# Performance work log

Hardware: AMD Instinct MI355X
Metric: run time of the kernel (lower is better)

The kernel has to match this reference:

```python
import jax, jax.numpy as jnp
import numpy as np

ROUTING_ITER = 2
EPS = 1e-8


def squash(s, axis):
    # s * ||s||^2 / (1 + ||s||^2) / ||s||
    sq = jnp.sum(s * s, axis=axis, keepdims=True)
    return s * (sq / (1.0 + sq)) / jnp.sqrt(sq + EPS)


def setup_inputs() -> dict:
    key = jax.random.key(0)
    k1, k2 = jax.random.split(key)
    B, N_in, d_in = 64, 2048, 16
    J, D = 32, 16  # num_capsule, dim_capsule
    x = jax.random.normal(k1, (B, N_in, 1, d_in), dtype=jnp.float32)
    weight = jax.random.normal(k2, (1, N_in, J, D, d_in), dtype=jnp.float32) * 0.05
    return {"x": x, "weight": weight}


def reference(x, weight):
    # x: [B, N_in, 1, d_in]; weight: [1, N_in, J, D, d_in]
    # prediction vectors u[b,i,j,:] = W[i,j] @ x[b,i]
    u = jnp.einsum('ijde,bie->bijd', weight[0], x[:, :, 0, :])  # [B,N_in,J,D]
    B, N_in, J, D = u.shape

    # dynamic routing on stop_gradient(u)
    u_sg = jax.lax.stop_gradient(u)
    b = jnp.zeros((B, N_in, J, 1), dtype=u.dtype)
    for _ in range(ROUTING_ITER):
        c = jax.nn.softmax(b, axis=2)                      # [B,N_in,J,1]
        s = jnp.sum(u_sg * c, axis=1, keepdims=True)       # [B,1,J,D]
        v = squash(s, axis=2)                              # squash over capsule axis (faithful)
        b = b + jnp.sum(u_sg * v, axis=-1, keepdims=True)  # [B,N_in,J,1]

    c = jax.nn.softmax(b, axis=2)
    s = jnp.sum(u * c, axis=1)  # [B,J,D]
    return squash(s, axis=-1)
```

## Files before the change

### kernel.cpp

```cpp
#include <hip/hip_runtime.h>

typedef __attribute__((ext_vector_type(8))) short short8;
typedef __attribute__((ext_vector_type(4))) float f32x4;
typedef __attribute__((ext_vector_type(2))) float f32x2;
typedef __attribute__((ext_vector_type(4))) unsigned int uint4v;
typedef unsigned short u16;

#define NI 2048

__device__ __forceinline__ unsigned int packbf2(float a, float b){
  unsigned int ua = __float_as_uint(a), ub = __float_as_uint(b);
  unsigned int ra = (ua + 0x7FFFu + ((ua >> 16) & 1u)) >> 16;
  unsigned int rb = (ub + 0x7FFFu + ((ub >> 16) & 1u)) & 0xFFFF0000u;
  return ra | rb;
}
__device__ __forceinline__ float bflo(unsigned int p){ return __uint_as_float(p << 16); }
__device__ __forceinline__ float bfhi(unsigned int p){ return __uint_as_float(p & 0xFFFF0000u); }

__device__ __forceinline__ uint4v cvt8(const f32x4& a, const f32x4& b){
  uint4v p = { packbf2(a.x, a.y), packbf2(a.z, a.w),
               packbf2(b.x, b.y), packbf2(b.z, b.w) };
  return p;
}

__device__ __forceinline__ void gl_lds16(const void* g, void* l){
  __builtin_amdgcn_global_load_lds(
      (const __attribute__((address_space(1))) unsigned int*)g,
      (__attribute__((address_space(3))) unsigned int*)l, 16, 0, 0);
}

__device__ __forceinline__ f32x4 squash4(const f32x4& q){
  f32x4 f;
  f.x = q.x / ((1.f + q.x) * sqrtf(q.x + 1e-8f));
  f.y = q.y / ((1.f + q.y) * sqrtf(q.y + 1e-8f));
  f.z = q.z / ((1.f + q.z) * sqrtf(q.z + 1e-8f));
  f.w = q.w / ((1.f + q.w) * sqrtf(q.w + 1e-8f));
  return f;
}


#define FUSED_SMEM 156672

template<int MODE>
__device__ __forceinline__ void pass_phase(
    const u16* __restrict__ sW, const u16* __restrict__ sX,
    float* __restrict__ sSumA, float* __restrict__ sSumB,
    const float* __restrict__ Sv1, const float* __restrict__ qv1,
    const float* __restrict__ Sv2, const float* __restrict__ qv2,
    float* __restrict__ partials, int blk, int t)
{
  const int w = t >> 6, lane = t & 63;
  const int wtile = w & 1, jhalf = (w >> 1) & 1, bh = w >> 2;
  const int lq = lane >> 4, lb = lane & 15, qs = lq & 1;
  const int bg = bh * 32 + wtile * 16 + lb;
  const short8 zero8 = {0,0,0,0,0,0,0,0};
  const f32x4 zf4 = {0.f,0.f,0.f,0.f};

  f32x4 acc[16];
  #pragma unroll
  for (int tj = 0; tj < 16; ++tj) acc[tj] = zf4;

  unsigned int vpl[16], vph[16];
  if constexpr (MODE >= 1){
    f32x4 qa = *(const f32x4*)(qv1 + bg * 16 + lq * 4);
    f32x4 fa = squash4(qa);
    f32x4 fb = zf4;
    if constexpr (MODE == 2){
      f32x4 qb = *(const f32x4*)(qv2 + bg * 16 + lq * 4);
      fb = squash4(qb);
    }
    #pragma unroll
    for (int tj = 0; tj < 16; ++tj){
      int jd = (jhalf * 16 + tj) * 16 + lq * 4;
      f32x4 sv = *(const f32x4*)(Sv1 + bg * 512 + jd);
      f32x4 v;
      v.x = sv.x * fa.x; v.y = sv.y * fa.y; v.z = sv.z * fa.z; v.w = sv.w * fa.w;
      if constexpr (MODE == 2){
        f32x4 s2 = *(const f32x4*)(Sv2 + bg * 512 + jd);
        v.x += s2.x * fb.x; v.y += s2.y * fb.y; v.z += s2.z * fb.z; v.w += s2.w * fb.w;
      }
      vpl[tj] = packbf2(v.x, v.y);
      vph[tj] = packbf2(v.z, v.w);
    }
  }

  if constexpr (MODE == 0){
    const int rsel = lq >> 1;
    #pragma unroll
    for (int s = 0; s < 4; ++s){
      const u16* wrow = sW + (size_t)(2 * s + rsel) * 8192;
      const u16* xrow = sX + (size_t)(2 * s + rsel) * 1024;
      short8 bfrag = *(const short8*)(xrow + bg * 16 + qs * 8);
      #pragma unroll
      for (int tj = 0; tj < 16; ++tj){
        int j = jhalf * 16 + tj;
        short8 afrag = *(const short8*)(wrow + j * 256 + lb * 16 + qs * 8);
        acc[tj] = __builtin_amdgcn_mfma_f32_16x16x32_bf16(afrag, bfrag, acc[tj], 0, 0, 0);
      }
    }
  } else {
    for (int s = 0; s < 8; ++s){
      const u16* wrow = sW + (size_t)s * 8192;
      const u16* xrow = sX + (size_t)s * 1024;
      short8 bl8 = *(const short8*)(xrow + bg * 16 + qs * 8);
      short8 bfrag = (lq < 2) ? bl8 : zero8;
      f32x4 ut[16];
      float e[16];
      float ps = 0.f;
      #pragma unroll
      for (int tj = 0; tj < 16; ++tj){
        int j = jhalf * 16 + tj;
        short8 afrag = *(const short8*)(wrow + j * 256 + lb * 16 + qs * 8);
        ut[tj] = __builtin_amdgcn_mfma_f32_16x16x32_bf16(afrag, bfrag, zf4, 0, 0, 0);
        float p = ut[tj].x * bflo(vpl[tj]) + ut[tj].y * bfhi(vpl[tj])
                + ut[tj].z * bflo(vph[tj]) + ut[tj].w * bfhi(vph[tj]);
        p += __shfl_xor(p, 16, 64);
        p += __shfl_xor(p, 32, 64);
        e[tj] = __expf(p);
        ps += e[tj];
      }
      float* sS = (s & 1) ? sSumB : sSumA;
      if (lane < 16) sS[w * 16 + lane] = ps;
      __syncthreads();
      float inv = 1.0f / (ps + sS[(w ^ 2) * 16 + lb]);
      #pragma unroll
      for (int tj = 0; tj < 16; ++tj){
        float c = e[tj] * inv;
        acc[tj].x += c * ut[tj].x;
        acc[tj].y += c * ut[tj].y;
        acc[tj].z += c * ut[tj].z;
        acc[tj].w += c * ut[tj].w;
      }
    }
  }

  float* dst = partials + ((size_t)blk * 8 + (size_t)w) * 4096 + (size_t)lane * 64;
  #pragma unroll
  for (int tj = 0; tj < 16; ++tj) *(f32x4*)(dst + tj * 4) = acc[tj];
}

__device__ __forceinline__ void reduce_phase(
    const float* __restrict__ partials, float* __restrict__ S,
    float* __restrict__ qbd, float* __restrict__ qbj,
    float scale, f32x4* __restrict__ sRed4, int blk, int t)
{
  const int qd = t & 31;
  const int dg = t >> 5;
  const float* src = partials + (size_t)dg * 16 * 32768 + (size_t)blk * 128 + qd * 4;
  f32x4 ld[16];
  #pragma unroll
  for (int p = 0; p < 16; ++p) ld[p] = *(const f32x4*)(src + (size_t)p * 32768);
  f32x4 a = ld[0];
  #pragma unroll
  for (int p = 1; p < 16; ++p){ a.x += ld[p].x; a.y += ld[p].y; a.z += ld[p].z; a.w += ld[p].w; }
  sRed4[t] = a;
  __syncthreads();
  if (t < 32){
    f32x4 s = sRed4[t];
    #pragma unroll
    for (int g = 1; g < 16; ++g){
      f32x4 r = sRed4[g * 32 + t];
      s.x += r.x; s.y += r.y; s.z += r.z; s.w += r.w;
    }
    s.x *= scale; s.y *= scale; s.z *= scale; s.w *= scale;
    const int oo = blk * 128 + t * 4;
    const int k = oo & 63, ln = (oo >> 6) & 63, wd = (oo >> 12) & 3, bh = oo >> 14;
    const int b = bh * 32 + (wd & 1) * 16 + (ln & 15);
    const int j = (wd >> 1) * 16 + (k >> 2);
    const int d0 = (ln >> 4) << 2;
    *(f32x4*)(S + b * 512 + j * 16 + d0) = s;
    if (qbd){
      atomicAdd(qbd + b * 16 + d0 + 0, s.x * s.x);
      atomicAdd(qbd + b * 16 + d0 + 1, s.y * s.y);
      atomicAdd(qbd + b * 16 + d0 + 2, s.z * s.z);
      atomicAdd(qbd + b * 16 + d0 + 3, s.w * s.w);
    }
    if (qbj) atomicAdd(qbj + b * 32 + j, s.x * s.x + s.y * s.y + s.z * s.z + s.w * s.w);
  }
  __syncthreads();
}

__global__ __launch_bounds__(512, 2)
void caps_fused(const float* __restrict__ X, const float* __restrict__ W,
                unsigned int* __restrict__ gcnt,
                float* __restrict__ qb1, float* __restrict__ qb2,
                float* __restrict__ qb3,
                float* __restrict__ S1, float* __restrict__ S2, float* __restrict__ S3,
                float* __restrict__ partials, float* __restrict__ out)
{
  extern __shared__ __align__(16) char smem[];
  u16* sW = (u16*)smem;
  u16* sX = (u16*)(smem + 131072);
  float* sSumA = (float*)(smem + 147456);
  float* sSumB = (float*)(smem + 147968);
  f32x4* sRed4 = (f32x4*)(smem + 148480);

  const int t = threadIdx.x;
  const int blk = blockIdx.x;
  const size_t i0 = (size_t)blk * 8;

  {
    const float* wsrc = W + i0 * 8192;
    #pragma unroll
    for (int k = 0; k < 16; ++k){
      int idx = k * 4096 + t * 8;
      f32x4 a = *(const f32x4*)(wsrc + idx);
      f32x4 b = *(const f32x4*)(wsrc + idx + 4);
      *(uint4v*)(sW + idx) = cvt8(a, b);
    }
    int r = t >> 6, b = t & 63;
    const float* xs = X + ((size_t)b * NI + i0 + (size_t)r) * 16;
    f32x4 a0 = *(const f32x4*)(xs);
    f32x4 a1 = *(const f32x4*)(xs + 4);
    f32x4 a2 = *(const f32x4*)(xs + 8);
    f32x4 a3 = *(const f32x4*)(xs + 12);
    *(uint4v*)(sX + t * 16)     = cvt8(a0, a1);
    *(uint4v*)(sX + t * 16 + 8) = cvt8(a2, a3);
  }
  __syncthreads();

  unsigned int gen = 0;
  auto gridsync = [&](bool wait){
    ++gen;
    __syncthreads();
    if (t == 0){
      __builtin_amdgcn_fence(__ATOMIC_RELEASE, "agent");
      __hip_atomic_fetch_add(gcnt + (blk & 7) * 4, 1u,
                             __ATOMIC_RELAXED, __HIP_MEMORY_SCOPE_AGENT);
      if (blk == 0){
        #pragma unroll 1
        for (int g = 0; g < 8; ++g){
          while (__hip_atomic_load(gcnt + g * 4, __ATOMIC_RELAXED,
                                   __HIP_MEMORY_SCOPE_AGENT) < gen * 32u)
            __builtin_amdgcn_s_sleep(2);
        }
        __builtin_amdgcn_fence(__ATOMIC_ACQ_REL, "agent");
        #pragma unroll
        for (int g = 0; g < 8; ++g)
          __hip_atomic_store(gcnt + 64 + g * 64, gen,
                             __ATOMIC_RELAXED, __HIP_MEMORY_SCOPE_AGENT);
      } else if (wait){
        while (__hip_atomic_load(gcnt + 64 + (blk & 7) * 64, __ATOMIC_RELAXED,
                                 __HIP_MEMORY_SCOPE_AGENT) < gen)
          __builtin_amdgcn_s_sleep(2);
        __builtin_amdgcn_fence(__ATOMIC_ACQUIRE, "agent");
      }
    }
    __syncthreads();
  };

  pass_phase<0>(sW, sX, sSumA, sSumB, nullptr, nullptr, nullptr, nullptr, partials, blk, t);
  gridsync(true);
  reduce_phase(partials, S1, qb1, nullptr, 1.0f / 32.0f, sRed4, blk, t);
  gridsync(true);

  pass_phase<1>(sW, sX, sSumA, sSumB, S1, qb1, nullptr, nullptr, partials, blk, t);
  gridsync(true);
  reduce_phase(partials, S2, qb2, nullptr, 1.0f, sRed4, blk, t);
  gridsync(true);

  pass_phase<2>(sW, sX, sSumA, sSumB, S1, qb1, S2, qb2, partials, blk, t);
  gridsync(true);
  reduce_phase(partials, S3, nullptr, qb3, 1.0f, sRed4, blk, t);
  gridsync(blk < 64);

  if (blk < 64){
    float s = S3[blk * 512 + t];
    float q = qb3[blk * 32 + (t >> 4)];
    out[blk * 512 + t] = s * (q / ((1.f + q) * sqrtf(q + 1e-8f)));
  }
}


__global__ __launch_bounds__(256)
void caps_prep(const float* __restrict__ W, const float* __restrict__ X,
               u16* __restrict__ Wb, u16* __restrict__ Xb)
{
  const int bid = blockIdx.x;
  if (bid < 8192){
    size_t base = (size_t)bid * 2048 + (size_t)threadIdx.x * 8;
    f32x4 a = *(const f32x4*)(W + base);
    f32x4 b = *(const f32x4*)(W + base + 4);
    *(uint4v*)(Wb + base) = cvt8(a, b);
  } else {
    int p = (bid - 8192) * 256 + threadIdx.x;
    int i = p >> 6, b = p & 63;
    const float* src = X + ((size_t)b * NI + i) * 16;
    f32x4 a0 = *(const f32x4*)(src);
    f32x4 a1 = *(const f32x4*)(src + 4);
    f32x4 a2 = *(const f32x4*)(src + 8);
    f32x4 a3 = *(const f32x4*)(src + 12);
    *(uint4v*)(Xb + (size_t)p * 16)     = cvt8(a0, a1);
    *(uint4v*)(Xb + (size_t)p * 16 + 8) = cvt8(a2, a3);
  }
}

template<int MODE>
__global__ __launch_bounds__(256, 2)
void caps_pass_f(const u16* __restrict__ Wb,
                 const u16* __restrict__ Xb,
                 const float* __restrict__ vbuf,
                 float* __restrict__ partials, int CI)
{
  constexpr int WR = (MODE == 0) ? 2 : 1;
  __shared__ __align__(16) u16 sW[2][WR * 8192];
  __shared__ __align__(16) u16 sX[2][WR * 512];
  __shared__ float sSum[4][16];

  const int t     = threadIdx.x;
  const int w     = t >> 6;
  const int lane  = t & 63;
  const int wtile = w & 1;
  const int jhalf = w >> 1;
  const int lq    = lane >> 4;
  const int lb    = lane & 15;
  const int q1    = lq & 1;
  const int bhalf = blockIdx.x & 1;
  const int iblk  = blockIdx.x >> 1;
  const int bloc  = wtile * 16 + lb;
  const int bg    = bhalf * 32 + bloc;
  const size_t i0 = (size_t)iblk * (size_t)CI;

  const short8 zero8 = {0,0,0,0,0,0,0,0};
  const f32x4  zf4   = {0.f,0.f,0.f,0.f};

  f32x4 acc[16];
  #pragma unroll
  for (int tj = 0; tj < 16; ++tj) acc[tj] = zf4;

  unsigned int vpl[16], vph[16];
  if constexpr (MODE == 1){
    #pragma unroll
    for (int tj = 0; tj < 16; ++tj){
      f32x4 v = *(const f32x4*)(&vbuf[bg * 512 + (jhalf * 16 + tj) * 16 + lq * 4]);
      vpl[tj] = packbf2(v.x, v.y);
      vph[tj] = packbf2(v.z, v.w);
    }
  }

  auto stage = [&](int nb, size_t irow){
    #pragma unroll
    for (int rr = 0; rr < WR; ++rr){
      const u16* src = Wb + (irow + rr) * 8192 + (size_t)(w * 4) * 512;
      u16* dst = &sW[nb][rr * 8192 + w * 4 * 512];
      #pragma unroll
      for (int r = 0; r < 4; ++r)
        gl_lds16(src + r * 512 + lane * 8, dst + r * 512);
    }
    if (w >= 4 - WR){
      int rr = w - (4 - WR);
      gl_lds16(Xb + ((irow + rr) * 64 + (size_t)bhalf * 32) * 16 + lane * 8,
               &sX[nb][rr * 512]);
    }
  };

  const int NSTEP = CI / WR;
  stage(0, i0);
  __syncthreads();

  for (int s = 0; s < NSTEP; ++s){
    const int buf = s & 1;
    if (s + 1 < NSTEP) stage(buf ^ 1, i0 + (size_t)(s + 1) * WR);

    if constexpr (MODE == 0){
      const int rsel = lq >> 1;
      short8 bfrag = *(const short8*)(&sX[buf][rsel * 512 + bloc * 16 + q1 * 8]);
      #pragma unroll
      for (int tj = 0; tj < 16; ++tj){
        int j = jhalf * 16 + tj;
        short8 afrag = *(const short8*)(&sW[buf][rsel * 8192 + j * 256 + lb * 16 + q1 * 8]);
        acc[tj] = __builtin_amdgcn_mfma_f32_16x16x32_bf16(afrag, bfrag, acc[tj], 0, 0, 0);
      }
    } else {
      short8 bl8 = *(const short8*)(&sX[buf][bloc * 16 + q1 * 8]);
      short8 bfrag = (lq < 2) ? bl8 : zero8;
      f32x4 ut[16];
      float e[16];
      float ps = 0.f;
      #pragma unroll
      for (int tj = 0; tj < 16; ++tj){
        int j = jhalf * 16 + tj;
        short8 al8 = *(const short8*)(&sW[buf][j * 256 + lb * 16 + q1 * 8]);
        short8 afrag = (lq < 2) ? al8 : zero8;
        ut[tj] = __builtin_amdgcn_mfma_f32_16x16x32_bf16(afrag, bfrag, zf4, 0, 0, 0);
        float p = ut[tj].x * bflo(vpl[tj]) + ut[tj].y * bfhi(vpl[tj])
                + ut[tj].z * bflo(vph[tj]) + ut[tj].w * bfhi(vph[tj]);
        p += __shfl_xor(p, 16, 64);
        p += __shfl_xor(p, 32, 64);
        e[tj] = __expf(p);
        ps += e[tj];
      }
      if (lane < 16) sSum[w][lane] = ps;
      __syncthreads();
      float inv = 1.0f / (ps + sSum[w ^ 2][lb]);
      #pragma unroll
      for (int tj = 0; tj < 16; ++tj){
        float c = e[tj] * inv;
        acc[tj].x += c * ut[tj].x;
        acc[tj].y += c * ut[tj].y;
        acc[tj].z += c * ut[tj].z;
        acc[tj].w += c * ut[tj].w;
      }
    }
    __syncthreads();
  }

  float* dst = partials + ((size_t)blockIdx.x * 4 + (size_t)w) * 4096 + (size_t)lane * 64;
  #pragma unroll
  for (int tj = 0; tj < 16; ++tj) *(f32x4*)(dst + tj * 4) = acc[tj];
}

template<int MODE>
__global__ __launch_bounds__(256)
void caps_pass_legacy(const float* __restrict__ Wg, const float* __restrict__ Xg,
                      const float* __restrict__ vbuf, float* __restrict__ partials, int CI)
{
  __shared__ __align__(16) unsigned short sW[2][8192];
  __shared__ __align__(16) unsigned int   sXd[2][256];
  __shared__ float sLog[(MODE == 1) ? (32 * 33) : 4];
  const int t = threadIdx.x, w = t >> 6, lane = t & 63;
  const int wtile = w & 1, jhalf = w >> 1, lq = lane >> 4, lb = lane & 15, q1 = lq & 1;
  const int bhalf = blockIdx.x & 1, iblk = blockIdx.x >> 1;
  const int bloc = wtile * 16 + lb, bg = bhalf * 32 + bloc;
  const size_t i0 = (size_t)iblk * (size_t)CI;
  const short8 zero8 = {0,0,0,0,0,0,0,0};
  const f32x4 zf4 = {0.f,0.f,0.f,0.f};
  f32x4 acc[16];
  #pragma unroll
  for (int tj = 0; tj < 16; ++tj) acc[tj] = zf4;
  unsigned int vpl[16], vph[16];
  if constexpr (MODE == 1){
    #pragma unroll
    for (int tj = 0; tj < 16; ++tj){
      f32x4 v = *(const f32x4*)(&vbuf[bg * 512 + (jhalf * 16 + tj) * 16 + lq * 4]);
      vpl[tj] = packbf2(v.x, v.y); vph[tj] = packbf2(v.z, v.w);
    }
  }
  {
    const float* wsrc = Wg + i0 * 8192;
    #pragma unroll
    for (int r = 0; r < 4; ++r){
      int c = r * 256 + t;
      f32x4 a = *(const f32x4*)(&wsrc[c * 8]);
      f32x4 b = *(const f32x4*)(&wsrc[c * 8 + 4]);
      *(uint4v*)(&sW[0][c * 8]) = cvt8(a, b);
    }
    int bidx = bhalf * 32 + (t >> 3), e2 = t & 7;
    f32x2 xv = *(const f32x2*)(&Xg[((size_t)bidx * NI + i0) * 16 + e2 * 2]);
    sXd[0][t] = packbf2(xv.x, xv.y);
  }
  __syncthreads();
  for (int s = 0; s < CI; ++s){
    const int buf = s & 1;
    f32x4 wpa[4], wpb[4]; f32x2 xp;
    const bool more = (s + 1 < CI);
    if (more){
      const float* wsrc = Wg + (i0 + (size_t)(s + 1)) * 8192;
      #pragma unroll
      for (int r = 0; r < 4; ++r){
        int c = r * 256 + t;
        wpa[r] = *(const f32x4*)(&wsrc[c * 8]);
        wpb[r] = *(const f32x4*)(&wsrc[c * 8 + 4]);
      }
      int bidx = bhalf * 32 + (t >> 3), e2 = t & 7;
      xp = *(const f32x2*)(&Xg[((size_t)bidx * NI + i0 + s + 1) * 16 + e2 * 2]);
    }
    const unsigned short* xrow = (const unsigned short*)&sXd[buf][0];
    short8 bl8 = *(const short8*)(&xrow[bloc * 16 + q1 * 8]);
    short8 bfrag = (lq < 2) ? bl8 : zero8;
    if constexpr (MODE == 0){
      #pragma unroll
      for (int tj = 0; tj < 16; ++tj){
        int j = jhalf * 16 + tj;
        short8 al8 = *(const short8*)(&sW[buf][j * 256 + lb * 16 + q1 * 8]);
        short8 afrag = (lq < 2) ? al8 : zero8;
        acc[tj] = __builtin_amdgcn_mfma_f32_16x16x32_bf16(afrag, bfrag, acc[tj], 0, 0, 0);
      }
    } else {
      #pragma unroll
      for (int tj = 0; tj < 16; ++tj){
        int j = jhalf * 16 + tj;
        short8 al8 = *(const short8*)(&sW[buf][j * 256 + lb * 16 + q1 * 8]);
        short8 afrag = (lq < 2) ? al8 : zero8;
        f32x4 u = __builtin_amdgcn_mfma_f32_16x16x32_bf16(afrag, bfrag, zf4, 0, 0, 0);
        float p = u.x * bflo(vpl[tj]) + u.y * bfhi(vpl[tj])
                + u.z * bflo(vph[tj]) + u.w * bfhi(vph[tj]);
        p += __shfl_xor(p, 16, 64);
        p += __shfl_xor(p, 32, 64);
        if (lane < 16) sLog[bloc * 33 + j] = p;
      }
      __syncthreads();
      const float* logrow = &sLog[bloc * 33];
      float ssum = 0.f;
      #pragma unroll
      for (int jj = 0; jj < 32; ++jj) ssum += __expf(logrow[jj]);
      float inv = 1.0f / ssum;
      #pragma unroll
      for (int tj = 0; tj < 16; ++tj){
        int j = jhalf * 16 + tj;
        short8 al8 = *(const short8*)(&sW[buf][j * 256 + lb * 16 + q1 * 8]);
        short8 afrag = (lq < 2) ? al8 : zero8;
        f32x4 u = __builtin_amdgcn_mfma_f32_16x16x32_bf16(afrag, bfrag, zf4, 0, 0, 0);
        float c = __expf(logrow[j]) * inv;
        acc[tj].x += c * u.x; acc[tj].y += c * u.y;
        acc[tj].z += c * u.z; acc[tj].w += c * u.w;
      }
    }
    if (more){
      const int nb = buf ^ 1;
      #pragma unroll
      for (int r = 0; r < 4; ++r){
        int c = r * 256 + t;
        *(uint4v*)(&sW[nb][c * 8]) = cvt8(wpa[r], wpb[r]);
      }
      sXd[nb][t] = packbf2(xp.x, xp.y);
    }
    __syncthreads();
  }
  float* dst = partials + ((size_t)blockIdx.x * 4 + (size_t)w) * 4096 + (size_t)lane * 64;
  #pragma unroll
  for (int tj = 0; tj < 16; ++tj) *(f32x4*)(dst + tj * 4) = acc[tj];
}

template<int NBLK>
__global__ __launch_bounds__(128)
void caps_reduce(const float* __restrict__ partials, float* __restrict__ S_buf, float scale)
{
  const int T = blockIdx.x * 128 + threadIdx.x;
  float s0 = 0.f, s1 = 0.f, s2 = 0.f, s3 = 0.f;
  #pragma unroll
  for (int bl = 0; bl < NBLK; bl += 4){
    s0 += partials[(size_t)(bl + 0) * 32768 + T];
    s1 += partials[(size_t)(bl + 1) * 32768 + T];
    s2 += partials[(size_t)(bl + 2) * 32768 + T];
    s3 += partials[(size_t)(bl + 3) * 32768 + T];
  }
  float s = ((s0 + s1) + (s2 + s3)) * scale;
  const int bhalf = T >> 14, w = (T >> 12) & 3, l = (T >> 6) & 63, k = T & 63;
  const int b  = bhalf * 32 + (w & 1) * 16 + (l & 15);
  const int jd = ((w >> 1) * 16 + (k >> 2)) * 16 + ((l >> 4) << 2) + (k & 3);
  S_buf[b * 512 + jd] = s;
}

__global__ __launch_bounds__(256)
void caps_squash_j(const float* __restrict__ S, const float* __restrict__ vprev,
                   float* __restrict__ vout)
{
  const int b = blockIdx.x, t = threadIdx.x;
  __shared__ float sq[16];
  if (t < 16) sq[t] = 0.f;
  __syncthreads();
  float s0 = S[b * 512 + t], s1 = S[b * 512 + 256 + t];
  atomicAdd(&sq[t & 15], s0 * s0 + s1 * s1);
  __syncthreads();
  float q = sq[t & 15];
  float f = q / ((1.f + q) * sqrtf(q + 1e-8f));
  float v0 = s0 * f, v1 = s1 * f;
  if (vprev){ v0 += vprev[b * 512 + t]; v1 += vprev[b * 512 + 256 + t]; }
  vout[b * 512 + t] = v0;
  vout[b * 512 + 256 + t] = v1;
}

__global__ __launch_bounds__(256)
void caps_squash_d(const float* __restrict__ S, float* __restrict__ out)
{
  const int b = blockIdx.x, t = threadIdx.x;
  __shared__ float sq[32];
  if (t < 32) sq[t] = 0.f;
  __syncthreads();
  float s0 = S[b * 512 + t], s1 = S[b * 512 + 256 + t];
  atomicAdd(&sq[t >> 4], s0 * s0);
  atomicAdd(&sq[(t + 256) >> 4], s1 * s1);
  __syncthreads();
  float q0 = sq[t >> 4], q1 = sq[(t + 256) >> 4];
  out[b * 512 + t]       = s0 * q0 / ((1.f + q0) * sqrtf(q0 + 1e-8f));
  out[b * 512 + 256 + t] = s1 * q1 / ((1.f + q1) * sqrtf(q1 + 1e-8f));
}

extern "C" void kernel_launch(void* const* d_in, const int* in_sizes, int n_in,
                              void* d_out, int out_size, void* d_ws, size_t ws_size,
                              hipStream_t stream)
{
  const float* X = (const float*)d_in[0];
  const float* W = (const float*)d_in[1];
  float* wsf = (float*)d_ws;

  const size_t OF_Q1   = 1024;
  const size_t OF_Q2   = OF_Q1 + 1024;
  const size_t OF_Q3   = OF_Q2 + 1024;
  const size_t OF_S1   = OF_Q3 + 2048;
  const size_t OF_S2   = OF_S1 + 32768;
  const size_t OF_S3   = OF_S2 + 32768;
  const size_t OF_PART = OF_S3 + 32768;
  const size_t FUSED_FLOATS = OF_PART + (size_t)256 * 32768;

  static int fused_ok = -1;
  if (fused_ok < 0){
    fused_ok = 0;
    hipFuncSetAttribute(reinterpret_cast<const void*>(caps_fused),
                        hipFuncAttributeMaxDynamicSharedMemorySize, FUSED_SMEM);
    int dev = 0, ncu = 0, nb = 0;
    hipGetDevice(&dev);
    hipDeviceGetAttribute(&ncu, hipDeviceAttributeMultiprocessorCount, dev);
    hipError_t e = hipOccupancyMaxActiveBlocksPerMultiprocessor(
        &nb, caps_fused, 512, (size_t)FUSED_SMEM);
    if (e == hipSuccess && nb >= 1 && ncu >= 256) fused_ok = 1;
  }

  if (fused_ok == 1 && ws_size >= FUSED_FLOATS * 4){
    hipMemsetAsync(d_ws, 0, (1024 + 1024 + 1024 + 2048) * 4, stream);
    caps_fused<<<dim3(256), dim3(512), FUSED_SMEM, stream>>>(
        X, W, (unsigned int*)wsf,
        wsf + OF_Q1, wsf + OF_Q2, wsf + OF_Q3,
        wsf + OF_S1, wsf + OF_S2, wsf + OF_S3, wsf + OF_PART, (float*)d_out);
    return;
  }

  const size_t FP = (size_t)256 * 32768;
  const size_t WB_ELE = (size_t)NI * 8192, XB_ELE = (size_t)NI * 64 * 16;
  const size_t need_full = (FP + 3 * 32768) * 4 + (WB_ELE + XB_ELE) * 2;

  if (ws_size >= need_full){
    float* partials = wsf;
    float* sbuf = wsf + FP;
    float* v1   = sbuf + 32768;
    float* v12  = v1 + 32768;
    u16* Wb = (u16*)(v12 + 32768);
    u16* Xb = Wb + WB_ELE;

    caps_prep<<<dim3(8704), dim3(256), 0, stream>>>(W, X, Wb, Xb);

    caps_pass_f<0><<<dim3(512), dim3(256), 0, stream>>>(Wb, Xb, nullptr, partials, 8);
    caps_reduce<256><<<dim3(256), dim3(128), 0, stream>>>(partials, sbuf, 1.0f / 32.0f);
    caps_squash_j<<<dim3(64), dim3(256), 0, stream>>>(sbuf, nullptr, v1);

    caps_pass_f<1><<<dim3(512), dim3(256), 0, stream>>>(Wb, Xb, v1, partials, 8);
    caps_reduce<256><<<dim3(256), dim3(128), 0, stream>>>(partials, sbuf, 1.0f);
    caps_squash_j<<<dim3(64), dim3(256), 0, stream>>>(sbuf, v1, v12);

    caps_pass_f<1><<<dim3(512), dim3(256), 0, stream>>>(Wb, Xb, v12, partials, 8);
    caps_reduce<256><<<dim3(256), dim3(128), 0, stream>>>(partials, sbuf, 1.0f);
    caps_squash_d<<<dim3(64), dim3(256), 0, stream>>>(sbuf, (float*)d_out);
  } else {
    int NBI = 256;
    auto need = [](int nb){ return ((size_t)nb * 32768 + 3 * 32768) * 4; };
    if (ws_size < need(256)){
      if      (ws_size >= need(64)) NBI = 64;
      else if (ws_size >= need(16)) NBI = 16;
      else                          NBI = 4;
    }
    const int CI = NI / NBI;
    float* partials = wsf;
    float* sbuf = wsf + (size_t)NBI * 32768;
    float* v1   = sbuf + 32768;
    float* v12  = v1 + 32768;
    auto reduce = [&](float scale){
      if      (NBI == 256) caps_reduce<256><<<dim3(256), dim3(128), 0, stream>>>(partials, sbuf, scale);
      else if (NBI ==  64) caps_reduce< 64><<<dim3(256), dim3(128), 0, stream>>>(partials, sbuf, scale);
      else if (NBI ==  16) caps_reduce< 16><<<dim3(256), dim3(128), 0, stream>>>(partials, sbuf, scale);
      else                 caps_reduce<  4><<<dim3(256), dim3(128), 0, stream>>>(partials, sbuf, scale);
    };
    caps_pass_legacy<0><<<dim3(2 * NBI), dim3(256), 0, stream>>>(W, X, nullptr, partials, CI);
    reduce(1.0f / 32.0f);
    caps_squash_j<<<dim3(64), dim3(256), 0, stream>>>(sbuf, nullptr, v1);
    caps_pass_legacy<1><<<dim3(2 * NBI), dim3(256), 0, stream>>>(W, X, v1, partials, CI);
    reduce(1.0f);
    caps_squash_j<<<dim3(64), dim3(256), 0, stream>>>(sbuf, v1, v12);
    caps_pass_legacy<1><<<dim3(2 * NBI), dim3(256), 0, stream>>>(W, X, v12, partials, CI);
    reduce(1.0f);
    caps_squash_d<<<dim3(64), dim3(256), 0, stream>>>(sbuf, (float*)d_out);
  }
}
```

Measured before the change: 234.1 us.

## Replace partials+reduce phases with global float atomics and lighter grid barriers

Each block now atomically adds its per-block accumulators directly into the S buffers instead of writing 256 partial slabs and running a separate grid-wide reduce phase. This removes two grid syncs per routing iteration and the large partials buffer traffic. The squared norms are then computed by 64 blocks with a two-level counter barrier, and the remaining blocks only wait on a flag. The cost is heavy contention on float atomics (256 blocks into 32K addresses) and a larger memset of the S buffers, plus nondeterministic summation order.

```diff
diff --git a/kernel.cpp b/kernel.cpp
--- a/kernel.cpp
+++ b/kernel.cpp
@@ -27,6 +27,20 @@
   __builtin_amdgcn_global_load_lds(
       (const __attribute__((address_space(1))) unsigned int*)g,
       (__attribute__((address_space(3))) unsigned int*)l, 16, 0, 0);
+}
+
+__device__ __forceinline__ void atadd4(float* p, f32x4 v){
+  asm volatile("global_atomic_add_f32 %0, %1, off\n\t"
+               "global_atomic_add_f32 %0, %2, off offset:4\n\t"
+               "global_atomic_add_f32 %0, %3, off offset:8\n\t"
+               "global_atomic_add_f32 %0, %4, off offset:12"
+               :: "v"(p), "v"(v.x), "v"(v.y), "v"(v.z), "v"(v.w) : "memory");
+}
+__device__ __forceinline__ void st4_coh(float* p, float v){
+  asm volatile("global_store_dword %0, %1, off sc1" :: "v"(p), "v"(v) : "memory");
+}
+__device__ __forceinline__ unsigned int spin_ld(const unsigned int* p){
+  return __hip_atomic_load(p, __ATOMIC_RELAXED, __HIP_MEMORY_SCOPE_AGENT);
 }
 
 __device__ __forceinline__ f32x4 squash4(const f32x4& q){
@@ -39,7 +53,7 @@
 }
 
 
-#define FUSED_SMEM 156672
+#define FUSED_SMEM 148608
 
 template<int MODE>
 __device__ __forceinline__ void pass_phase(
@@ -47,7 +61,7 @@
     float* __restrict__ sSumA, float* __restrict__ sSumB,
     const float* __restrict__ Sv1, const float* __restrict__ qv1,
     const float* __restrict__ Sv2, const float* __restrict__ qv2,
-    float* __restrict__ partials, int blk, int t)
+    float* __restrict__ Sout, float scale, int blk, int t)
 {
   const int w = t >> 6, lane = t & 63;
   const int wtile = w & 1, jhalf = (w >> 1) & 1, bh = w >> 2;
@@ -134,66 +148,27 @@
     }
   }
 
-  float* dst = partials + ((size_t)blk * 8 + (size_t)w) * 4096 + (size_t)lane * 64;
   #pragma unroll
-  for (int tj = 0; tj < 16; ++tj) *(f32x4*)(dst + tj * 4) = acc[tj];
-}
-
-__device__ __forceinline__ void reduce_phase(
-    const float* __restrict__ partials, float* __restrict__ S,
-    float* __restrict__ qbd, float* __restrict__ qbj,
-    float scale, f32x4* __restrict__ sRed4, int blk, int t)
-{
-  const int qd = t & 31;
-  const int dg = t >> 5;
-  const float* src = partials + (size_t)dg * 16 * 32768 + (size_t)blk * 128 + qd * 4;
-  f32x4 ld[16];
-  #pragma unroll
-  for (int p = 0; p < 16; ++p) ld[p] = *(const f32x4*)(src + (size_t)p * 32768);
-  f32x4 a = ld[0];
-  #pragma unroll
-  for (int p = 1; p < 16; ++p){ a.x += ld[p].x; a.y += ld[p].y; a.z += ld[p].z; a.w += ld[p].w; }
-  sRed4[t] = a;
-  __syncthreads();
-  if (t < 32){
-    f32x4 s = sRed4[t];
-    #pragma unroll
-    for (int g = 1; g < 16; ++g){
-      f32x4 r = sRed4[g * 32 + t];
-      s.x += r.x; s.y += r.y; s.z += r.z; s.w += r.w;
-    }
-    s.x *= scale; s.y *= scale; s.z *= scale; s.w *= scale;
-    const int oo = blk * 128 + t * 4;
-    const int k = oo & 63, ln = (oo >> 6) & 63, wd = (oo >> 12) & 3, bh = oo >> 14;
-    const int b = bh * 32 + (wd & 1) * 16 + (ln & 15);
-    const int j = (wd >> 1) * 16 + (k >> 2);
-    const int d0 = (ln >> 4) << 2;
-    *(f32x4*)(S + b * 512 + j * 16 + d0) = s;
-    if (qbd){
-      atomicAdd(qbd + b * 16 + d0 + 0, s.x * s.x);
-      atomicAdd(qbd + b * 16 + d0 + 1, s.y * s.y);
-      atomicAdd(qbd + b * 16 + d0 + 2, s.z * s.z);
-      atomicAdd(qbd + b * 16 + d0 + 3, s.w * s.w);
-    }
-    if (qbj) atomicAdd(qbj + b * 32 + j, s.x * s.x + s.y * s.y + s.z * s.z + s.w * s.w);
-  }
-  __syncthreads();
+  for (int tj = 0; tj < 16; ++tj){
+    f32x4 v = acc[tj];
+    v.x *= scale; v.y *= scale; v.z *= scale; v.w *= scale;
+    atadd4(Sout + bg * 512 + (jhalf * 16 + tj) * 16 + lq * 4, v);
+  }
 }
 
 __global__ __launch_bounds__(512, 2)
 void caps_fused(const float* __restrict__ X, const float* __restrict__ W,
-                unsigned int* __restrict__ gcnt,
-                float* __restrict__ qb1, float* __restrict__ qb2,
-                float* __restrict__ qb3,
+                unsigned int* __restrict__ cnt,
+                float* __restrict__ q1, float* __restrict__ q2,
                 float* __restrict__ S1, float* __restrict__ S2, float* __restrict__ S3,
-                float* __restrict__ partials, float* __restrict__ out)
+                float* __restrict__ out)
 {
   extern __shared__ __align__(16) char smem[];
   u16* sW = (u16*)smem;
   u16* sX = (u16*)(smem + 131072);
   float* sSumA = (float*)(smem + 147456);
   float* sSumB = (float*)(smem + 147968);
-  f32x4* sRed4 = (f32x4*)(smem + 148480);
+  float* sq    = (float*)(smem + 148480);
 
   const int t = threadIdx.x;
   const int blk = blockIdx.x;
@@ -219,55 +194,88 @@
   }
   __syncthreads();
 
-  unsigned int gen = 0;
-  auto gridsync = [&](bool wait){
-    ++gen;
+  auto barrier_qstage = [&](int s, const float* Ssrc, float* qdst){
+    asm volatile("s_waitcnt vmcnt(0)" ::: "memory");
     __syncthreads();
-    if (t == 0){
-      __builtin_amdgcn_fence(__ATOMIC_RELEASE, "agent");
-      __hip_atomic_fetch_add(gcnt + (blk & 7) * 4, 1u,
-                             __ATOMIC_RELAXED, __HIP_MEMORY_SCOPE_AGENT);
-      if (blk == 0){
+    if (blk < 64){
+      if (t == 0){
+        __hip_atomic_fetch_add(cnt + s * 8 + (blk & 7), 1u,
+                               __ATOMIC_RELAXED, __HIP_MEMORY_SCOPE_AGENT);
         #pragma unroll 1
-        for (int g = 0; g < 8; ++g){
-          while (__hip_atomic_load(gcnt + g * 4, __ATOMIC_RELAXED,
-                                   __HIP_MEMORY_SCOPE_AGENT) < gen * 32u)
+        for (int g = 0; g < 8; ++g)
+          while (spin_ld(cnt + s * 8 + g) < 32u) __builtin_amdgcn_s_sleep(2);
+        __builtin_amdgcn_fence(__ATOMIC_ACQUIRE, "agent");
+      }
+      __syncthreads();
+      float sv_ = Ssrc[blk * 512 + t];
+      if (t < 16) sq[t] = 0.f;
+      __syncthreads();
+      atomicAdd(&sq[t & 15], sv_ * sv_);
+      __syncthreads();
+      if (t < 16) st4_coh(qdst + blk * 16 + t, sq[t]);
+      asm volatile("s_waitcnt vmcnt(0)" ::: "memory");
+      __syncthreads();
+      if (t == 0){
+        __hip_atomic_fetch_add(cnt + 32 + s * 8 + (blk & 7), 1u,
+                               __ATOMIC_RELAXED, __HIP_MEMORY_SCOPE_AGENT);
+        if (blk == 0){
+          #pragma unroll 1
+          for (int g = 0; g < 8; ++g)
+            while (spin_ld(cnt + 32 + s * 8 + g) < 8u) __builtin_amdgcn_s_sleep(2);
+          #pragma unroll
+          for (int g = 0; g < 8; ++g)
+            __hip_atomic_store(cnt + 128 + s * 128 + g * 16, 1u,
+                               __ATOMIC_RELAXED, __HIP_MEMORY_SCOPE_AGENT);
+        } else {
+          while (spin_ld(cnt + 128 + s * 128 + (blk & 7) * 16) == 0u)
             __builtin_amdgcn_s_sleep(2);
         }
-        __builtin_amdgcn_fence(__ATOMIC_ACQ_REL, "agent");
-        #pragma unroll
-        for (int g = 0; g < 8; ++g)
-          __hip_atomic_store(gcnt + 64 + g * 64, gen,
-                             __ATOMIC_RELAXED, __HIP_MEMORY_SCOPE_AGENT);
-      } else if (wait){
-        while (__hip_atomic_load(gcnt + 64 + (blk & 7) * 64, __ATOMIC_RELAXED,
-                                 __HIP_MEMORY_SCOPE_AGENT) < gen)
+        __builtin_amdgcn_fence(__ATOMIC_ACQUIRE, "agent");
+      }
+      __syncthreads();
+    } else {
+      if (t == 0){
+        __hip_atomic_fetch_add(cnt + s * 8 + (blk & 7), 1u,
+                               __ATOMIC_RELAXED, __HIP_MEMORY_SCOPE_AGENT);
+        while (spin_ld(cnt + 128 + s * 128 + (blk & 7) * 16) == 0u)
           __builtin_amdgcn_s_sleep(2);
         __builtin_amdgcn_fence(__ATOMIC_ACQUIRE, "agent");
       }
+      __syncthreads();
+    }
+  };
+
+  pass_phase<0>(sW, sX, sSumA, sSumB, nullptr, nullptr, nullptr, nullptr,
+                S1, 1.0f / 32.0f, blk, t);
+  barrier_qstage(0, S1, q1);
+
+  pass_phase<1>(sW, sX, sSumA, sSumB, S1, q1, nullptr, nullptr,
+                S2, 1.0f, blk, t);
+  barrier_qstage(1, S2, q2);
+
+  pass_phase<2>(sW, sX, sSumA, sSumB, S1, q1, S2, q2,
+                S3, 1.0f, blk, t);
+
+  asm volatile("s_waitcnt vmcnt(0)" ::: "memory");
+  __syncthreads();
+  if (t == 0)
+    __hip_atomic_fetch_add(cnt + 16 + (blk & 7), 1u,
+                           __ATOMIC_RELAXED, __HIP_MEMORY_SCOPE_AGENT);
+  if (blk < 64){
+    if (t == 0){
+      #pragma unroll 1
+      for (int g = 0; g < 8; ++g)
+        while (spin_ld(cnt + 16 + g) < 32u) __builtin_amdgcn_s_sleep(2);
+      __builtin_amdgcn_fence(__ATOMIC_ACQUIRE, "agent");
     }
     __syncthreads();
-  };
-
-  pass_phase<0>(sW, sX, sSumA, sSumB, nullptr, nullptr, nullptr, nullptr, partials, blk, t);
-  gridsync(true);
-  reduce_phase(partials, S1, qb1, nullptr, 1.0f / 32.0f, sRed4, blk, t);
-  gridsync(true);
-
-  pass_phase<1>(sW, sX, sSumA, sSumB, S1, qb1, nullptr, nullptr, partials, blk, t);
-  gridsync(true);
-  reduce_phase(partials, S2, qb2, nullptr, 1.0f, sRed4, blk, t);
-  gridsync(true);
-
-  pass_phase<2>(sW, sX, sSumA, sSumB, S1, qb1, S2, qb2, partials, blk, t);
-  gridsync(true);
-  reduce_phase(partials, S3, nullptr, qb3, 1.0f, sRed4, blk, t);
-  gridsync(blk < 64);
-
-  if (blk < 64){
-    float s = S3[blk * 512 + t];
-    float q = qb3[blk * 32 + (t >> 4)];
-    out[blk * 512 + t] = s * (q / ((1.f + q) * sqrtf(q + 1e-8f)));
+    float sv_ = S3[blk * 512 + t];
+    if (t < 32) sq[t] = 0.f;
+    __syncthreads();
+    atomicAdd(&sq[t >> 4], sv_ * sv_);
+    __syncthreads();
+    float qq = sq[t >> 4];
+    out[blk * 512 + t] = sv_ * (qq / ((1.f + qq) * sqrtf(qq + 1e-8f)));
   }
 }
 
@@ -585,14 +593,12 @@
   const float* W = (const float*)d_in[1];
   float* wsf = (float*)d_ws;
 
-  const size_t OF_Q1   = 1024;
-  const size_t OF_Q2   = OF_Q1 + 1024;
-  const size_t OF_Q3   = OF_Q2 + 1024;
-  const size_t OF_S1   = OF_Q3 + 2048;
-  const size_t OF_S2   = OF_S1 + 32768;
-  const size_t OF_S3   = OF_S2 + 32768;
-  const size_t OF_PART = OF_S3 + 32768;
-  const size_t FUSED_FLOATS = OF_PART + (size_t)256 * 32768;
+  const size_t OF_Q1 = 1024;
+  const size_t OF_Q2 = OF_Q1 + 1024;
+  const size_t OF_S1 = OF_Q2 + 1024;
+  const size_t OF_S2 = OF_S1 + 32768;
+  const size_t OF_S3 = OF_S2 + 32768;
+  const size_t FUSED_FLOATS = OF_S3 + 32768;
 
   static int fused_ok = -1;
   if (fused_ok < 0){
@@ -608,11 +614,11 @@
   }
 
   if (fused_ok == 1 && ws_size >= FUSED_FLOATS * 4){
-    hipMemsetAsync(d_ws, 0, (1024 + 1024 + 1024 + 2048) * 4, stream);
+    hipMemsetAsync(d_ws, 0, FUSED_FLOATS * 4, stream);
     caps_fused<<<dim3(256), dim3(512), FUSED_SMEM, stream>>>(
         X, W, (unsigned int*)wsf,
-        wsf + OF_Q1, wsf + OF_Q2, wsf + OF_Q3,
-        wsf + OF_S1, wsf + OF_S2, wsf + OF_S3, wsf + OF_PART, (float*)d_out);
+        wsf + OF_Q1, wsf + OF_Q2,
+        wsf + OF_S1, wsf + OF_S2, wsf + OF_S3, (float*)d_out);
     return;
   }
 
```

Result: no change. 232.0 us (-0.9%).
